# Kernel optimization log

Hardware: AMD Instinct MI355X
Metric: run time of the kernel (lower is better)

## Reference

```python
import jax, jax.numpy as jnp
import numpy as np

DIM = 768
NUM_PROMPTS = 10
LATENT = 20
B = 16
N = 4096
EPS = 1e-5


def quick_gelu(x):
    return x * jax.nn.sigmoid(1.702 * x)


def layer_norm(x, g, b):
    mu = jnp.mean(x, axis=-1, keepdims=True)
    var = jnp.var(x, axis=-1, keepdims=True)
    return (x - mu) * jax.lax.rsqrt(var + EPS) * g + b


def setup_inputs() -> dict:
    key = jax.random.key(0)
    ks = jax.random.split(key, 12)
    s_in = 1.0 / np.sqrt(DIM)
    s_lat = 1.0 / np.sqrt(LATENT)
    s64 = 1.0 / np.sqrt(64)
    return {
        "x": jax.random.normal(ks[0], (B, NUM_PROMPTS + 1 + N, DIM), jnp.float32),
        "local_tokens": jax.random.normal(ks[1], (B, N, DIM), jnp.float32),
        # proj_down: Linear(dim, latent)
        "Wd": jax.random.uniform(ks[2], (DIM, LATENT), jnp.float32, -s_in, s_in),
        "bd": jnp.zeros((LATENT,), jnp.float32),
        # proj_up: Linear(latent, dim)
        "Wu": jax.random.uniform(ks[3], (LATENT, DIM), jnp.float32, -s_lat, s_lat),
        "bu": jnp.zeros((DIM,), jnp.float32),
        # global / local query projections: Linear(latent, latent)
        "Wgq": jax.random.uniform(ks[4], (LATENT, LATENT), jnp.float32, -s_lat, s_lat),
        "bgq": jnp.zeros((LATENT,), jnp.float32),
        "Wlq": jax.random.uniform(ks[5], (LATENT, LATENT), jnp.float32, -s_lat, s_lat),
        "blq": jnp.zeros((LATENT,), jnp.float32),
        # cls_analyzer: LN(latent) -> Linear(latent,64) -> GELU -> Linear(64,num_prompts) -> Sigmoid
        "ln_c_g": jnp.ones((LATENT,), jnp.float32),
        "ln_c_b": jnp.zeros((LATENT,), jnp.float32),
        "Wc1": jax.random.uniform(ks[6], (LATENT, 64), jnp.float32, -s_lat, s_lat),
        "bc1": jnp.zeros((64,), jnp.float32),
        "Wc2": jax.random.uniform(ks[7], (64, NUM_PROMPTS), jnp.float32, -s64, s64),
        "bc2": jnp.zeros((NUM_PROMPTS,), jnp.float32),
        # gl_balancer: LN(latent) -> Linear(latent,1) -> Sigmoid
        "ln_g_g": jnp.ones((LATENT,), jnp.float32),
        "ln_g_b": jnp.zeros((LATENT,), jnp.float32),
        "Wg": jax.random.uniform(ks[8], (LATENT, 1), jnp.float32, -s_lat, s_lat),
        "bg": jnp.zeros((1,), jnp.float32),
    }


def _attend(q, tokens, scale):
    # q: [B,P,d], tokens: [B,n,d]
    w = jax.nn.softmax(jnp.einsum('bpd,bnd->bpn', q, tokens) * scale, axis=-1)
    return jnp.einsum('bpn,bnd->bpd', w, tokens)


def reference(x, local_tokens, Wd, bd, Wu, bu, Wgq, bgq, Wlq, blq,
              ln_c_g, ln_c_b, Wc1, bc1, Wc2, bc2, ln_g_g, ln_g_b, Wg, bg):
    scale = LATENT ** (-0.5)
    x_latent = quick_gelu(x @ Wd + bd)            # [B, P+1+N, d]
    local_latent = quick_gelu(local_tokens @ Wd + bd)  # [B, N, d]

    prompts_latent = x_latent[:, :NUM_PROMPTS]              # [B,P,d]
    cls_latent = x_latent[:, NUM_PROMPTS:NUM_PROMPTS + 1]   # [B,1,d]
    global_img_latent = x_latent[:, NUM_PROMPTS + 1:]       # [B,N,d]

    cls_ln = layer_norm(cls_latent, ln_c_g, ln_c_b)
    prompt_importance = jax.nn.sigmoid(
        jax.nn.gelu(cls_ln @ Wc1 + bc1, approximate=False) @ Wc2 + bc2)  # [B,1,P]
    global_weight = jax.nn.sigmoid(layer_norm(cls_latent, ln_g_g, ln_g_b) @ Wg + bg)  # [B,1,1]

    global_context = _attend(prompts_latent @ Wgq + bgq, global_img_latent, scale)
    local_context = _attend(prompts_latent @ Wlq + blq, local_latent, scale)

    fused = global_weight * global_context + (1.0 - global_weight) * local_context
    enhanced = fused * jnp.swapaxes(prompt_importance, 1, 2)  # [B,P,d]

    combined = jnp.concatenate([enhanced, cls_latent, global_img_latent], axis=1)
    return combined @ Wu + bu
```

## Files before the change

kernel.cpp:

```cpp
#include <hip/hip_runtime.h>
#include <math.h>

#define DIM   768
#define LAT   20
#define NP    10
#define NB    16
#define SEQ   4096
#define SEQX  (NP + 1 + SEQ)
#define NXROWS (NB * SEQX)
#define NLROWS (NB * SEQ)
#define NROWS  (NXROWS + NLROWS)
#define EPSF  1e-5f

__device__ __forceinline__ float sigmoidf_(float z) { return 1.f / (1.f + __expf(-z)); }

__global__ __launch_bounds__(256) void k_down(const float* __restrict__ x,
                                              const float* __restrict__ loc,
                                              const float* __restrict__ Wd,
                                              const float* __restrict__ bd,
                                              float* __restrict__ lat)
{
    __shared__ float wds[DIM * LAT];
    {
        const float4* s = (const float4*)Wd;
        float4* d = (float4*)wds;
        for (int i = threadIdx.x; i < DIM * LAT / 4; i += 256) d[i] = s[i];
    }
    __syncthreads();

    int row = blockIdx.x * 256 + threadIdx.x;
    if (row >= NROWS) return;
    const float* src = (row < NXROWS) ? (x + (size_t)row * DIM)
                                      : (loc + (size_t)(row - NXROWS) * DIM);
    float acc[LAT];
#pragma unroll
    for (int j = 0; j < LAT; j++) acc[j] = 0.f;

    for (int k = 0; k < DIM; k += 4) {
        float4 xv = *(const float4*)(src + k);
#pragma unroll
        for (int j = 0; j < LAT; j++) acc[j] += xv.x * wds[(k + 0) * LAT + j];
#pragma unroll
        for (int j = 0; j < LAT; j++) acc[j] += xv.y * wds[(k + 1) * LAT + j];
#pragma unroll
        for (int j = 0; j < LAT; j++) acc[j] += xv.z * wds[(k + 2) * LAT + j];
#pragma unroll
        for (int j = 0; j < LAT; j++) acc[j] += xv.w * wds[(k + 3) * LAT + j];
    }

    float outv[LAT];
#pragma unroll
    for (int j = 0; j < LAT; j++) {
        float z = acc[j] + bd[j];
        outv[j] = z * sigmoidf_(1.702f * z);
    }
    float4* dst = (float4*)(lat + (size_t)row * LAT);
#pragma unroll
    for (int i = 0; i < LAT / 4; i++) dst[i] = ((float4*)outv)[i];
}

__global__ __launch_bounds__(192) void k_up(const float* __restrict__ lat,
                                            const float* __restrict__ Wu,
                                            const float* __restrict__ bu,
                                            float* __restrict__ out)
{
    int t = threadIdx.x;
    float4 wu[LAT];
#pragma unroll
    for (int k = 0; k < LAT; k++) wu[k] = ((const float4*)Wu)[k * 192 + t];
    float4 bv = ((const float4*)bu)[t];

    int rowbase = blockIdx.x * 64;
    for (int i = 0; i < 64; i++) {
        int row = rowbase + i;
        if (row >= NXROWS) return;
        int idx = row % SEQX;
        if (idx < NP) continue;
        const float* lp = lat + (size_t)row * LAT;
        float4 acc = bv;
#pragma unroll
        for (int k = 0; k < LAT; k++) {
            float l = lp[k];
            acc.x += l * wu[k].x; acc.y += l * wu[k].y;
            acc.z += l * wu[k].z; acc.w += l * wu[k].w;
        }
        ((float4*)out)[(size_t)row * 192 + t] = acc;
    }
}

__global__ __launch_bounds__(64) void k_small(const float* __restrict__ lat_x,
    const float* __restrict__ Wgq, const float* __restrict__ bgq,
    const float* __restrict__ Wlq, const float* __restrict__ blq,
    const float* __restrict__ lncg, const float* __restrict__ lncb,
    const float* __restrict__ Wc1, const float* __restrict__ bc1,
    const float* __restrict__ Wc2, const float* __restrict__ bc2,
    const float* __restrict__ lngg, const float* __restrict__ lngb,
    const float* __restrict__ Wg, const float* __restrict__ bg,
    float* __restrict__ qg, float* __restrict__ ql,
    float* __restrict__ imp, float* __restrict__ gw)
{
    int b = blockIdx.x, t = threadIdx.x;
    __shared__ float cls[LAT], clsln[LAT], h1[64];
    __shared__ float mu_s, rs_s;

    const float* cp = lat_x + (size_t)(b * SEQX + NP) * LAT;
    if (t < LAT) cls[t] = cp[t];
    __syncthreads();

    if (t == 0) {
        float m = 0.f;
        for (int k = 0; k < LAT; k++) m += cls[k];
        m /= LAT;
        float v = 0.f;
        for (int k = 0; k < LAT; k++) { float d = cls[k] - m; v += d * d; }
        v /= LAT;
        float rs = rsqrtf(v + EPSF);
        mu_s = m; rs_s = rs;
        float s = bg[0];
        for (int k = 0; k < LAT; k++)
            s += ((cls[k] - m) * rs * lngg[k] + lngb[k]) * Wg[k];
        gw[b] = sigmoidf_(s);
    }
    __syncthreads();
    if (t < LAT) clsln[t] = (cls[t] - mu_s) * rs_s * lncg[t] + lncb[t];
    __syncthreads();

    {
        float s = bc1[t];
        for (int k = 0; k < LAT; k++) s += clsln[k] * Wc1[k * 64 + t];
        h1[t] = 0.5f * s * (1.f + erff(s * 0.70710678118f));
    }
    __syncthreads();
    if (t < NP) {
        float s = bc2[t];
        for (int i = 0; i < 64; i++) s += h1[i] * Wc2[i * NP + t];
        imp[b * NP + t] = sigmoidf_(s);
    }
    for (int idx = t; idx < NP * LAT; idx += 64) {
        int p = idx / LAT, j = idx % LAT;
        const float* pl = lat_x + (size_t)(b * SEQX + p) * LAT;
        float sg = bgq[j], sl = blq[j];
        for (int k = 0; k < LAT; k++) {
            float v = pl[k];
            sg += v * Wgq[k * LAT + j];
            sl += v * Wlq[k * LAT + j];
        }
        qg[(b * NP + p) * LAT + j] = sg;
        ql[(b * NP + p) * LAT + j] = sl;
    }
}

__global__ __launch_bounds__(256) void k_attn(const float* __restrict__ lat_x,
                                              const float* __restrict__ lat_l,
                                              const float* __restrict__ qg,
                                              const float* __restrict__ ql,
                                              float* __restrict__ ctxg,
                                              float* __restrict__ ctxl)
{
    int b = blockIdx.x, p = blockIdx.y, ty = blockIdx.z;
    const float* tok = (ty == 0) ? lat_x + (size_t)(b * SEQX + NP + 1) * LAT
                                 : lat_l + (size_t)b * SEQ * LAT;
    const float* q = ((ty == 0) ? qg : ql) + (size_t)(b * NP + p) * LAT;
    float* ctx = ((ty == 0) ? ctxg : ctxl) + (size_t)(b * NP + p) * LAT;

    int t = threadIdx.x;
    __shared__ float qs[LAT];
    __shared__ float red[128];
    __shared__ float Ms;
    __shared__ float tot[21];
    if (t < LAT) qs[t] = q[t];
    __syncthreads();

    const float scale = 0.22360679775f;
    float lg[16];
    float lmax = -1e30f;
    for (int i = 0; i < 16; i++) {
        const float* tk = tok + (size_t)(t + 256 * i) * LAT;
        float s = 0.f;
#pragma unroll
        for (int k = 0; k < LAT; k++) s += qs[k] * tk[k];
        s *= scale;
        lg[i] = s;
        lmax = fmaxf(lmax, s);
    }
    int wave = t >> 6, lane = t & 63;
    for (int off = 32; off; off >>= 1) lmax = fmaxf(lmax, __shfl_down(lmax, off, 64));
    if (lane == 0) red[wave] = lmax;
    __syncthreads();
    if (t == 0) Ms = fmaxf(fmaxf(red[0], red[1]), fmaxf(red[2], red[3]));
    __syncthreads();
    float M = Ms;

    float vals[21];
#pragma unroll
    for (int j = 0; j < 21; j++) vals[j] = 0.f;
    for (int i = 0; i < 16; i++) {
        float w = __expf(lg[i] - M);
        vals[20] += w;
        const float* tk = tok + (size_t)(t + 256 * i) * LAT;
#pragma unroll
        for (int k = 0; k < LAT; k++) vals[k] += w * tk[k];
    }
#pragma unroll
    for (int j = 0; j < 21; j++) {
        float v = vals[j];
        for (int off = 32; off; off >>= 1) v += __shfl_down(v, off, 64);
        vals[j] = v;
    }
    __syncthreads();
    if (lane == 0)
        for (int j = 0; j < 21; j++) red[wave * 21 + j] = vals[j];
    __syncthreads();
    if (t < 21) tot[t] = red[t] + red[21 + t] + red[42 + t] + red[63 + t];
    __syncthreads();
    if (t < LAT) ctx[t] = tot[t] / tot[20];
}

__global__ __launch_bounds__(192) void k_prompt_out(const float* __restrict__ ctxg,
                                                    const float* __restrict__ ctxl,
                                                    const float* __restrict__ imp,
                                                    const float* __restrict__ gw,
                                                    const float* __restrict__ Wu,
                                                    const float* __restrict__ bu,
                                                    float* __restrict__ out)
{
    int b = blockIdx.x, p = blockIdx.y, t = threadIdx.x;
    __shared__ float enh[LAT];
    if (t < LAT) {
        float g = gw[b];
        size_t o = (size_t)(b * NP + p) * LAT + t;
        float e = g * ctxg[o] + (1.f - g) * ctxl[o];
        enh[t] = e * imp[b * NP + p];
    }
    __syncthreads();
    float4 acc = ((const float4*)bu)[t];
#pragma unroll
    for (int k = 0; k < LAT; k++) {
        float4 w = ((const float4*)Wu)[k * 192 + t];
        float e = enh[k];
        acc.x += e * w.x; acc.y += e * w.y; acc.z += e * w.z; acc.w += e * w.w;
    }
    ((float4*)out)[(size_t)(b * SEQX + p) * 192 + t] = acc;
}

extern "C" void kernel_launch(void* const* d_in, const int* in_sizes, int n_in,
                              void* d_out, int out_size, void* d_ws, size_t ws_size,
                              hipStream_t stream)
{
    const float* x    = (const float*)d_in[0];
    const float* loc  = (const float*)d_in[1];
    const float* Wd   = (const float*)d_in[2];
    const float* bd   = (const float*)d_in[3];
    const float* Wu   = (const float*)d_in[4];
    const float* bu   = (const float*)d_in[5];
    const float* Wgq  = (const float*)d_in[6];
    const float* bgq  = (const float*)d_in[7];
    const float* Wlq  = (const float*)d_in[8];
    const float* blq  = (const float*)d_in[9];
    const float* lncg = (const float*)d_in[10];
    const float* lncb = (const float*)d_in[11];
    const float* Wc1  = (const float*)d_in[12];
    const float* bc1  = (const float*)d_in[13];
    const float* Wc2  = (const float*)d_in[14];
    const float* bc2  = (const float*)d_in[15];
    const float* lngg = (const float*)d_in[16];
    const float* lngb = (const float*)d_in[17];
    const float* Wg   = (const float*)d_in[18];
    const float* bg   = (const float*)d_in[19];
    float* out = (float*)d_out;

    float* ws   = (float*)d_ws;
    float* lat_x = ws;
    float* lat_l = lat_x + (size_t)NXROWS * LAT;
    float* qg    = lat_l + (size_t)NLROWS * LAT;
    float* ql    = qg + NB * NP * LAT;
    float* ctxg  = ql + NB * NP * LAT;
    float* ctxl  = ctxg + NB * NP * LAT;
    float* impw  = ctxl + NB * NP * LAT;
    float* gww   = impw + NB * NP;

    k_down<<<(NROWS + 255) / 256, 256, 0, stream>>>(x, loc, Wd, bd, lat_x);
    k_up<<<(NXROWS + 63) / 64, 192, 0, stream>>>(lat_x, Wu, bu, out);
    k_small<<<NB, 64, 0, stream>>>(lat_x, Wgq, bgq, Wlq, blq, lncg, lncb,
                                   Wc1, bc1, Wc2, bc2, lngg, lngb, Wg, bg,
                                   qg, ql, impw, gww);
    k_attn<<<dim3(NB, NP, 2), 256, 0, stream>>>(lat_x, lat_l, qg, ql, ctxg, ctxl);
    k_prompt_out<<<dim3(NB, NP), 192, 0, stream>>>(ctxg, ctxl, impw, gww, Wu, bu, out);
}
```

Baseline: 661.7 us.

## Use bf16 MFMA for down-projection with double-buffered LDS staging

Rewrites the down-projection from a per-thread fp32 scalar dot product into a tiled GEMM. It converts input rows and Wd to bf16 in LDS and runs 16x16x32 bf16 MFMA instructions, with double-buffered staging of 128-column chunks. The up-projection kernel now loads its 64-row latent tile into shared memory once and replaces the per-row modulo with an incremental index. The aim is to cut the VALU-bound compute of the old down kernel. The cost is reduced precision from bf16 rounding of both the activations and the weights.

```diff
diff --git a/kernel.cpp b/kernel.cpp
--- a/kernel.cpp
+++ b/kernel.cpp
@@ -12,57 +12,112 @@
 #define NROWS  (NXROWS + NLROWS)
 #define EPSF  1e-5f
 
+typedef __attribute__((ext_vector_type(8))) short  v8s;
+typedef __attribute__((ext_vector_type(4))) float  v4f;
+typedef __attribute__((ext_vector_type(4))) unsigned short u16x4;
+typedef __attribute__((ext_vector_type(8))) unsigned short u16x8;
+
 __device__ __forceinline__ float sigmoidf_(float z) { return 1.f / (1.f + __expf(-z)); }
 
-__global__ __launch_bounds__(256) void k_down(const float* __restrict__ x,
-                                              const float* __restrict__ loc,
-                                              const float* __restrict__ Wd,
-                                              const float* __restrict__ bd,
-                                              float* __restrict__ lat)
-{
-    __shared__ float wds[DIM * LAT];
-    {
-        const float4* s = (const float4*)Wd;
-        float4* d = (float4*)wds;
-        for (int i = threadIdx.x; i < DIM * LAT / 4; i += 256) d[i] = s[i];
-    }
-    __syncthreads();
-
-    int row = blockIdx.x * 256 + threadIdx.x;
-    if (row >= NROWS) return;
-    const float* src = (row < NXROWS) ? (x + (size_t)row * DIM)
-                                      : (loc + (size_t)(row - NXROWS) * DIM);
-    float acc[LAT];
-#pragma unroll
-    for (int j = 0; j < LAT; j++) acc[j] = 0.f;
-
-    for (int k = 0; k < DIM; k += 4) {
-        float4 xv = *(const float4*)(src + k);
-#pragma unroll
-        for (int j = 0; j < LAT; j++) acc[j] += xv.x * wds[(k + 0) * LAT + j];
-#pragma unroll
-        for (int j = 0; j < LAT; j++) acc[j] += xv.y * wds[(k + 1) * LAT + j];
-#pragma unroll
-        for (int j = 0; j < LAT; j++) acc[j] += xv.z * wds[(k + 2) * LAT + j];
-#pragma unroll
-        for (int j = 0; j < LAT; j++) acc[j] += xv.w * wds[(k + 3) * LAT + j];
-    }
-
-    float outv[LAT];
-#pragma unroll
-    for (int j = 0; j < LAT; j++) {
-        float z = acc[j] + bd[j];
-        outv[j] = z * sigmoidf_(1.702f * z);
-    }
-    float4* dst = (float4*)(lat + (size_t)row * LAT);
-#pragma unroll
-    for (int i = 0; i < LAT / 4; i++) dst[i] = ((float4*)outv)[i];
-}
-
-__global__ __launch_bounds__(192) void k_up(const float* __restrict__ lat,
-                                            const float* __restrict__ Wu,
-                                            const float* __restrict__ bu,
-                                            float* __restrict__ out)
+__device__ __forceinline__ unsigned short bf16u(float v) {
+    unsigned u = __builtin_bit_cast(unsigned, v);
+    unsigned r = u + 0x7fffu + ((u >> 16) & 1u);
+    return (unsigned short)(r >> 16);
+}
+
+#define WF_US   24576
+#define XBUF_US 8192
+__global__ __launch_bounds__(256, 2) void k_down(const float* __restrict__ x,
+                                                 const float* __restrict__ loc,
+                                                 const float* __restrict__ Wd,
+                                                 const float* __restrict__ bd,
+                                                 float* __restrict__ lat)
+{
+    __shared__ __align__(16) unsigned short lds[WF_US + 2 * XBUF_US];
+    const int tid = threadIdx.x;
+    const int rowbase = blockIdx.x * 64;
+
+    for (int slot = tid; slot < 3072; slot += 256) {
+        int fs = slot >> 7;
+        int rem = slot & 127;
+        int nt = rem >> 6, l = rem & 63;
+        int n = nt * 16 + (l & 15);
+        int q = l >> 4;
+        u16x8 w;
+#pragma unroll
+        for (int e = 0; e < 8; e++) {
+            int k = fs * 32 + q * 8 + e;
+            float v = (n < LAT) ? Wd[k * LAT + n] : 0.f;
+            w[e] = bf16u(v);
+        }
+        *(u16x8*)&lds[((fs * 2 + nt) * 64 + l) * 8] = w;
+    }
+
+    auto stage = [&](int c, int b) {
+        const int base = WF_US + b * XBUF_US;
+#pragma unroll
+        for (int i = 0; i < 8; i++) {
+            int g = tid + 256 * i;
+            int row_l = g >> 5, fq = g & 31;
+            int kc = fq << 2;
+            int row = rowbase + row_l;
+            float4 f = make_float4(0.f, 0.f, 0.f, 0.f);
+            if (row < NROWS) {
+                const float* src = (row < NXROWS) ? x + (size_t)row * DIM
+                                                  : loc + (size_t)(row - NXROWS) * DIM;
+                f = *(const float4*)(src + c * 128 + kc);
+            }
+            int s = kc >> 5, q = (kc >> 3) & 3, e = kc & 7;
+            int t = row_l >> 4, m = row_l & 15;
+            int lane = q * 16 + m;
+            u16x4 u = { bf16u(f.x), bf16u(f.y), bf16u(f.z), bf16u(f.w) };
+            *(u16x4*)&lds[base + ((s * 4 + t) * 64 + lane) * 8 + e] = u;
+        }
+    };
+
+    stage(0, 0);
+    __syncthreads();
+
+    const int t = tid >> 6, l = tid & 63;
+    v4f acc0 = {0.f, 0.f, 0.f, 0.f}, acc1 = {0.f, 0.f, 0.f, 0.f};
+
+    for (int c = 0; c < 6; c++) {
+        if (c < 5) stage(c + 1, (c + 1) & 1);
+        const int base = WF_US + (c & 1) * XBUF_US;
+#pragma unroll
+        for (int s = 0; s < 4; s++) {
+            v8s a  = *(const v8s*)&lds[base + ((s * 4 + t) * 64 + l) * 8];
+            int fs = c * 4 + s;
+            v8s b0 = *(const v8s*)&lds[((fs * 2 + 0) * 64 + l) * 8];
+            v8s b1 = *(const v8s*)&lds[((fs * 2 + 1) * 64 + l) * 8];
+            acc0 = __builtin_amdgcn_mfma_f32_16x16x32_bf16(a, b0, acc0, 0, 0, 0);
+            acc1 = __builtin_amdgcn_mfma_f32_16x16x32_bf16(a, b1, acc1, 0, 0, 0);
+        }
+        __syncthreads();
+    }
+
+    int col = l & 15, half = l >> 4;
+#pragma unroll
+    for (int nt = 0; nt < 2; nt++) {
+        int j = nt * 16 + col;
+        if (j >= LAT) continue;
+        float bdj = bd[j];
+        v4f A = nt ? acc1 : acc0;
+#pragma unroll
+        for (int r = 0; r < 4; r++) {
+            int rowg = rowbase + t * 16 + half * 4 + r;
+            if (rowg < NROWS) {
+                float z = A[r] + bdj;
+                lat[(size_t)rowg * LAT + j] = z * sigmoidf_(1.702f * z);
+            }
+        }
+    }
+}
+
+__global__ __launch_bounds__(192, 3) void k_up(const float* __restrict__ lat,
+                                               const float* __restrict__ Wu,
+                                               const float* __restrict__ bu,
+                                               float* __restrict__ out)
 {
     int t = threadIdx.x;
     float4 wu[LAT];
@@ -70,19 +125,28 @@
     for (int k = 0; k < LAT; k++) wu[k] = ((const float4*)Wu)[k * 192 + t];
     float4 bv = ((const float4*)bu)[t];
 
+    __shared__ float latile[64 * LAT];
     int rowbase = blockIdx.x * 64;
+    {
+        const float4* src = (const float4*)(lat + (size_t)rowbase * LAT);
+        for (int idx = t; idx < 320; idx += 192) ((float4*)latile)[idx] = src[idx];
+    }
+    __syncthreads();
+
+    int idx0 = rowbase % SEQX;
     for (int i = 0; i < 64; i++) {
         int row = rowbase + i;
-        if (row >= NXROWS) return;
-        int idx = row % SEQX;
+        if (row >= NXROWS) break;
+        int idx = idx0 + i;
+        if (idx >= SEQX) idx -= SEQX;
         if (idx < NP) continue;
-        const float* lp = lat + (size_t)row * LAT;
+        const float* lp = latile + i * LAT;
         float4 acc = bv;
 #pragma unroll
         for (int k = 0; k < LAT; k++) {
-            float l = lp[k];
-            acc.x += l * wu[k].x; acc.y += l * wu[k].y;
-            acc.z += l * wu[k].z; acc.w += l * wu[k].w;
+            float v = lp[k];
+            acc.x += v * wu[k].x; acc.y += v * wu[k].y;
+            acc.z += v * wu[k].z; acc.w += v * wu[k].w;
         }
         ((float4*)out)[(size_t)row * 192 + t] = acc;
     }
@@ -279,7 +343,7 @@
     float* impw  = ctxl + NB * NP * LAT;
     float* gww   = impw + NB * NP;
 
-    k_down<<<(NROWS + 255) / 256, 256, 0, stream>>>(x, loc, Wd, bd, lat_x);
+    k_down<<<(NROWS + 63) / 64, 256, 0, stream>>>(x, loc, Wd, bd, lat_x);
     k_up<<<(NXROWS + 63) / 64, 192, 0, stream>>>(lat_x, Wu, bu, out);
     k_small<<<NB, 64, 0, stream>>>(lat_x, Wgq, bgq, Wlq, blq, lncg, lncb,
                                    Wc1, bc1, Wc2, bc2, lngg, lngb, Wg, bg,
```

Result: faster. 640.9 us (-3.2%).
